# Kernel optimization log

Hardware: AMD Instinct MI355X
Metric: run time of the kernel (lower is better)

The kernel has to match this reference:

```python
import jax, jax.numpy as jnp
import numpy as np
from jax import lax

DIM = 256
HEADS = 8


def dwconv3x3(x, w, b):
    # x: [B,C,H,W], w: [C,1,3,3] depthwise (groups=C), b: [C]
    y = lax.conv_general_dilated(
        x, w, window_strides=(1, 1), padding='SAME',
        dimension_numbers=('NCHW', 'OIHW', 'NCHW'),
        feature_group_count=x.shape[1])
    return y + b[None, :, None, None]


def conv1x1(x, w, b):
    # x: [B,Cin,H,W], w: [Cout,Cin], b: [Cout]
    return jnp.einsum('oc,bchw->bohw', w, x) + b[None, :, None, None]


def setup_inputs() -> dict:
    key = jax.random.key(0)
    ks = jax.random.split(key, 12)
    s = 0.05
    inp = {
        'x': jax.random.normal(ks[0], (4, DIM, 128, 128), dtype=jnp.float32),
        'q_w': jax.random.normal(ks[1], (DIM, 1, 3, 3), dtype=jnp.float32) * s,
        'q_b': jax.random.normal(ks[2], (DIM,), dtype=jnp.float32) * s,
        'k_w': jax.random.normal(ks[3], (DIM, 1, 3, 3), dtype=jnp.float32) * s,
        'k_b': jax.random.normal(ks[4], (DIM,), dtype=jnp.float32) * s,
        'v_w': jax.random.normal(ks[5], (DIM, 1, 3, 3), dtype=jnp.float32) * s,
        'v_b': jax.random.normal(ks[6], (DIM,), dtype=jnp.float32) * s,
        'out_w': jax.random.normal(ks[7], (DIM, DIM), dtype=jnp.float32) * s,
        'out_b': jax.random.normal(ks[8], (DIM,), dtype=jnp.float32) * s,
        'fusion_w': jax.random.normal(ks[9], (DIM, 2 * DIM), dtype=jnp.float32) * s,
        'fusion_b': jax.random.normal(ks[10], (DIM,), dtype=jnp.float32) * s,
        'temperature': jnp.ones((HEADS, 1, 1), dtype=jnp.float32),
        'gamma': jax.random.normal(ks[11], (1,), dtype=jnp.float32) * 0.1,
    }
    return inp


def reference(x, q_w, q_b, k_w, k_b, v_w, v_b, out_w, out_b,
              fusion_w, fusion_b, temperature, gamma):
    b, c, h, w = x.shape
    ch = c // HEADS  # channels per head (32)
    q = dwconv3x3(x, q_w, q_b).reshape(b, HEADS, ch, h * w)
    k = dwconv3x3(x, k_w, k_b).reshape(b, HEADS, ch, h * w)
    v = dwconv3x3(x, v_w, v_b).reshape(b, HEADS, ch, h * w)
    # channel-wise attention: [b, head, c, c]
    attn = jnp.einsum('bhcn,bhdn->bhcd', q, k) * temperature[None]
    attn = jax.nn.softmax(attn, axis=-1)
    out = jnp.einsum('bhcd,bhdn->bhcn', attn, v).reshape(b, c, h, w)
    out = conv1x1(out, out_w, out_b)
    fused = jnp.concatenate([out * gamma[0], x], axis=1)  # [b, 2c, h, w]
    return conv1x1(fused, fusion_w, fusion_b)
```

## Files before the change

kernel.cpp:

```cpp
#include <hip/hip_runtime.h>

typedef __attribute__((ext_vector_type(8))) short bf16x8;
typedef __attribute__((ext_vector_type(4))) float f32x4;

static __device__ __forceinline__ unsigned short f2bf(float f) {
  unsigned u = __builtin_bit_cast(unsigned, f);
  unsigned r = u + 0x7fffu + ((u >> 16) & 1u);
  return (unsigned short)(r >> 16);
}
static __device__ __forceinline__ unsigned pkbf(float a, float b) {
  return (unsigned)f2bf(a) | ((unsigned)f2bf(b) << 16);
}

#define GLOAD_LDS16(g, l)                                              \
  __builtin_amdgcn_global_load_lds(                                    \
      (const __attribute__((address_space(1))) void*)(g),              \
      (__attribute__((address_space(3))) void*)(l), 16, 0, 0)

struct SmA { float xs[4][324]; unsigned short qk[2][32][256]; };
union SmU { SmA a; unsigned short vx[256][72]; };

__global__ __launch_bounds__(256, 4) void k_qkv(
    const float* __restrict__ x,
    const float* __restrict__ q_w, const float* __restrict__ q_b,
    const float* __restrict__ k_w, const float* __restrict__ k_b,
    const float* __restrict__ v_w, const float* __restrict__ v_b,
    unsigned short* __restrict__ bx,
    float* __restrict__ gp)
{
  __shared__ SmU sm;
  const int lin = blockIdx.x + 64 * (blockIdx.y + 8 * blockIdx.z);
  const int nl = ((lin & 7) << 8) | (lin >> 3);
  const int t = nl & 63, h = (nl >> 6) & 7, b = nl >> 9;
  const int tid = threadIdx.x;
  __builtin_assume(tid < 256);
  const int wv = tid >> 6, lane = tid & 63;
  const int w4 = __builtin_amdgcn_readfirstlane(wv);
  const int ty = t >> 3, tx = t & 7;
  const int y0 = ty * 16, x0 = tx * 16;
  const int py = lane >> 2, px0 = (lane & 3) * 4;

  int goff[6];
  #pragma unroll
  for (int k = 0; k < 6; ++k) {
    int r = lane + 64 * k;
    int yy = r / 18, xx = r - yy * 18;
    int gy = y0 + yy - 1, gx = x0 + xx - 1;
    goff[k] = ((r < 324) && ((unsigned)gy < 128u) && ((unsigned)gx < 128u))
                  ? (gy * 128 + gx) : -1;
  }
  const float* cb = x + ((size_t)(b * 256 + h * 32 + w4 * 4)) * 16384;
  float hc[6], hn[6];
  #pragma unroll
  for (int k = 0; k < 6; ++k) { hc[k] = 0.f; if (goff[k] >= 0) hc[k] = cb[goff[k]]; }

  float* xw = &sm.a.xs[w4][0];
  uint2 vpack[2][4], xpack[2][4];
  #pragma unroll
  for (int pass = 0; pass < 2; ++pass) {
    const int cbase = h * 32 + pass * 16;
    #pragma unroll
    for (int j = 0; j < 4; ++j) {
      #pragma unroll
      for (int k = 0; k < 6; ++k) {
        int r = lane + 64 * k;
        if (r < 324) xw[r] = hc[k];
      }
      const bool last = (pass == 1) && (j == 3);
      const int nrel = (j < 3) ? (pass * 16 + j + 1) : 16;
      if (!last) {
        const float* np = cb + (size_t)nrel * 16384;
        #pragma unroll
        for (int k = 0; k < 6; ++k) { hn[k] = 0.f; if (goff[k] >= 0) hn[k] = np[goff[k]]; }
      }
      const int ch = cbase + w4 * 4 + j;
      float wq[9], wk[9], wvv[9];
      #pragma unroll
      for (int i2 = 0; i2 < 9; ++i2) {
        wq[i2]  = q_w[ch * 9 + i2];
        wk[i2]  = k_w[ch * 9 + i2];
        wvv[i2] = v_w[ch * 9 + i2];
      }
      const float bq = q_b[ch], bk = k_b[ch], bv = v_b[ch];
      float aq[4], ak[4], av[4], xr[4];
      #pragma unroll
      for (int px = 0; px < 4; ++px) { aq[px] = bq; ak[px] = bk; av[px] = bv; xr[px] = 0.f; }
      #pragma unroll
      for (int r = 0; r < 3; ++r) {
        const float* xrow = &xw[(py + r) * 18 + px0];
        float2 a01 = *(const float2*)&xrow[0];
        float2 a23 = *(const float2*)&xrow[2];
        float2 a45 = *(const float2*)&xrow[4];
        float rw[6];
        rw[0] = a01.x; rw[1] = a01.y; rw[2] = a23.x;
        rw[3] = a23.y; rw[4] = a45.x; rw[5] = a45.y;
        #pragma unroll
        for (int px = 0; px < 4; ++px) {
          #pragma unroll
          for (int cx = 0; cx < 3; ++cx) {
            float xv = rw[px + cx];
            aq[px] += wq[r * 3 + cx] * xv;
            ak[px] += wk[r * 3 + cx] * xv;
            av[px] += wvv[r * 3 + cx] * xv;
          }
        }
        if (r == 1) {
          #pragma unroll
          for (int px = 0; px < 4; ++px) xr[px] = rw[px + 1];
        }
      }
      const int ah = pass * 16 + w4 * 4 + j;
      const int sw = (((lane >> 1) ^ (ah & 7)) << 3) + ((lane & 1) << 2);
      *(uint2*)&sm.a.qk[0][ah][sw] = make_uint2(pkbf(aq[0], aq[1]), pkbf(aq[2], aq[3]));
      *(uint2*)&sm.a.qk[1][ah][sw] = make_uint2(pkbf(ak[0], ak[1]), pkbf(ak[2], ak[3]));
      #pragma unroll
      for (int px = 0; px < 4; ++px) {
        unsigned fv = (unsigned)f2bf(av[px]);
        unsigned fx = (unsigned)f2bf(xr[px]);
        if (j == 0)      { vpack[pass][px].x = fv;        xpack[pass][px].x = fx; }
        else if (j == 1) { vpack[pass][px].x |= fv << 16; xpack[pass][px].x |= fx << 16; }
        else if (j == 2) { vpack[pass][px].y = fv;        xpack[pass][px].y = fx; }
        else             { vpack[pass][px].y |= fv << 16; xpack[pass][px].y |= fx << 16; }
      }
      if (!last) {
        #pragma unroll
        for (int k = 0; k < 6; ++k) hc[k] = hn[k];
      }
    }
  }
  __syncthreads();

  const int qm = wv >> 1, qn = wv & 1;
  const int lrow = lane & 15, quad = lane >> 4;
  const int rowa = qm * 16 + lrow, rowb = qn * 16 + lrow;
  f32x4 acc = {0.f, 0.f, 0.f, 0.f};
  #pragma unroll
  for (int ks = 0; ks < 8; ++ks) {
    bf16x8 a  = *(const bf16x8*)&sm.a.qk[0][rowa][(((ks * 4 + quad) ^ (rowa & 7)) << 3)];
    bf16x8 bb = *(const bf16x8*)&sm.a.qk[1][rowb][(((ks * 4 + quad) ^ (rowb & 7)) << 3)];
    acc = __builtin_amdgcn_mfma_f32_16x16x32_bf16(a, bb, acc, 0, 0, 0);
  }
  float* gpb = gp + ((size_t)((b * 8 + h) * 64 + t)) * 1024;
  #pragma unroll
  for (int r = 0; r < 4; ++r)
    gpb[(qm * 16 + quad * 4 + r) * 32 + qn * 16 + lrow] = acc[r];

  __syncthreads();

  const int chi = wv >> 1, half = wv & 1;
  #pragma unroll
  for (int pass = 0; pass < 2; ++pass)
    #pragma unroll
    for (int px = 0; px < 4; ++px) {
      int n = py * 16 + px0 + px;
      int key = (n >> 3) & 7;
      int cv = pass * 2 + chi;
      int cx2 = 4 + pass * 2 + chi;
      *(uint2*)&sm.vx[n][((cv ^ key) << 3) + (half << 2)] = vpack[pass][px];
      *(uint2*)&sm.vx[n][((cx2 ^ key) << 3) + (half << 2)] = xpack[pass][px];
    }
  __syncthreads();

  #pragma unroll
  for (int it = 0; it < 8; ++it) {
    int n = it * 32 + (tid >> 3);
    int m = tid & 7;
    int key = (n >> 3) & 7;
    uint4 val = *(const uint4*)&sm.vx[n][((m ^ key) << 3)];
    int pyn = n >> 4, pxn = n & 15;
    int ng = (y0 + pyn) * 128 + x0 + pxn;
    *(uint4*)&bx[((size_t)b * 16384 + ng) * 512 + h * 64 + m * 8] = val;
  }
}

__global__ __launch_bounds__(256) void k_rs_prep(
    const float* __restrict__ gp, const float* __restrict__ temp,
    float* __restrict__ attn,
    const float* __restrict__ out_w, const float* __restrict__ out_b,
    const float* __restrict__ fusion_w, const float* __restrict__ fusion_b,
    const float* __restrict__ gamma,
    float* __restrict__ W1g, float* __restrict__ bias_tot,
    unsigned short* __restrict__ Wcat) {
  const int bi = blockIdx.x;
  const int tid = threadIdx.x;

  if (bi >= 128) {
    const int o = bi - 128;
    const int c = tid;
    const float g = gamma[0];
    float acc = 0.f, bacc = 0.f;
    #pragma unroll 8
    for (int t = 0; t < 256; ++t) {
      float fw = fusion_w[o*512 + t];
      acc  += fw * out_w[t*256 + c];
      bacc += fw * out_b[t];
    }
    W1g[o*256 + c] = g * acc;
    if (c == 0) bias_tot[o] = g * bacc + fusion_b[o];
    unsigned short w2b = f2bf(fusion_w[o*512 + 256 + c]);
    const int col = ((c >> 5) << 6) + 32 + (c & 31);
    for (int b = 0; b < 4; ++b)
      Wcat[((size_t)(b*256 + o))*512 + col] = w2b;
    return;
  }

  const int cs = bi & 3, h = (bi >> 2) & 7, b = bi >> 5;
  const int lc = tid >> 5, d = tid & 31;
  const int c = cs * 8 + lc;
  const float* base = gp + ((size_t)((b*8 + h)*64))*1024 + c*32 + d;
  float s = 0.f;
  #pragma unroll
  for (int g = 0; g < 8; ++g) {
    float p = 0.f;
    #pragma unroll
    for (int i = 0; i < 8; ++i) p += base[(size_t)(g*8 + i)*1024];
    s += p;
  }
  s *= temp[h];
  float m = s;
  #pragma unroll
  for (int off = 16; off; off >>= 1) m = fmaxf(m, __shfl_xor(m, off));
  float e = __expf(s - m);
  float sum = e;
  #pragma unroll
  for (int off = 16; off; off >>= 1) sum += __shfl_xor(sum, off);
  attn[((size_t)((b*8 + h)*32 + c))*32 + d] = e / sum;
}

__global__ __launch_bounds__(256) void k_compose(
    const float* __restrict__ W1g, const float* __restrict__ attn,
    unsigned short* __restrict__ Wcat) {
  const int o = blockIdx.x, b = blockIdx.y;
  const int e = threadIdx.x;
  const int h = e >> 5, d = e & 31;
  const float* ab = attn + ((size_t)((b*8 + h)*32))*32 + d;
  const float* wb = W1g + o*256 + h*32;
  float s = 0.f;
  #pragma unroll
  for (int c2 = 0; c2 < 32; ++c2) s += wb[c2] * ab[c2*32];
  Wcat[((size_t)(b*256 + o))*512 + ((e >> 5) << 6) + (e & 31)] = f2bf(s);
}

__global__ __launch_bounds__(256) void k_gemm(
    const unsigned short* __restrict__ Wcat,
    const unsigned short* __restrict__ bx,
    const float* __restrict__ bias_tot,
    float* __restrict__ out) {
  __shared__ unsigned short Al[2][256][32];
  __shared__ unsigned short Bl[2][64][32];
  const int nt = blockIdx.x, b = blockIdx.y;
  const int tid = threadIdx.x;
  const int wv = tid >> 6, lane = tid & 63;
  const int lrow = lane & 15, quad = lane >> 4;
  const int nbase = nt * 64;
  const unsigned short* Ab = Wcat + (size_t)b * 256 * 512;
  const unsigned short* Bb = bx + ((size_t)b * 16384 + nbase) * 512;
  f32x4 acc[4][4] = {};

  const int srow = tid >> 2;
  const int sq4 = tid & 3;
  const unsigned short* apr = Ab + (size_t)srow * 512 + sq4 * 8;
  const unsigned short* bpr = Bb + (size_t)srow * 512 + sq4 * 8;

  #pragma unroll
  for (int g = 0; g < 4; ++g)
    GLOAD_LDS16(apr + (size_t)g * 64 * 512, &Al[0][wv * 16 + g * 64][0]);
  GLOAD_LDS16(bpr, &Bl[0][wv * 16][0]);
  __syncthreads();

  for (int ks = 0; ks < 16; ++ks) {
    const int cur = ks & 1;
    if (ks < 15) {
      const int k0 = (ks + 1) * 32;
      const int nxt = cur ^ 1;
      #pragma unroll
      for (int g = 0; g < 4; ++g)
        GLOAD_LDS16(apr + (size_t)g * 64 * 512 + k0, &Al[nxt][wv * 16 + g * 64][0]);
      GLOAD_LDS16(bpr + k0, &Bl[nxt][wv * 16][0]);
    }
    bf16x8 af[4], bfv[4];
    #pragma unroll
    for (int i = 0; i < 4; ++i)
      af[i] = *(const bf16x8*)&Al[cur][wv * 64 + i * 16 + lrow][quad * 8];
    #pragma unroll
    for (int j = 0; j < 4; ++j)
      bfv[j] = *(const bf16x8*)&Bl[cur][j * 16 + lrow][quad * 8];
    #pragma unroll
    for (int i = 0; i < 4; ++i)
      #pragma unroll
      for (int j = 0; j < 4; ++j)
        acc[i][j] = __builtin_amdgcn_mfma_f32_16x16x32_bf16(af[i], bfv[j], acc[i][j], 0, 0, 0);
    __syncthreads();
  }

  #pragma unroll
  for (int i = 0; i < 4; ++i) {
    #pragma unroll
    for (int r = 0; r < 4; ++r) {
      const int o = wv*64 + i*16 + quad*4 + r;
      const float bias = bias_tot[o];
      #pragma unroll
      for (int j = 0; j < 4; ++j) {
        const int n = nbase + j*16 + lrow;
        out[((size_t)(b*256 + o))*16384 + n] = acc[i][j][r] + bias;
      }
    }
  }
}

extern "C" void kernel_launch(void* const* d_in, const int* in_sizes, int n_in,
                              void* d_out, int out_size, void* d_ws, size_t ws_size,
                              hipStream_t stream) {
  const float* x        = (const float*)d_in[0];
  const float* q_w      = (const float*)d_in[1];
  const float* q_b      = (const float*)d_in[2];
  const float* k_w      = (const float*)d_in[3];
  const float* k_b      = (const float*)d_in[4];
  const float* v_w      = (const float*)d_in[5];
  const float* v_b      = (const float*)d_in[6];
  const float* out_w    = (const float*)d_in[7];
  const float* out_b    = (const float*)d_in[8];
  const float* fusion_w = (const float*)d_in[9];
  const float* fusion_b = (const float*)d_in[10];
  const float* temp     = (const float*)d_in[11];
  const float* gamma    = (const float*)d_in[12];
  float* out = (float*)d_out;

  char* ws = (char*)d_ws;
  unsigned short* bx   = (unsigned short*)(ws);
  float* gp            = (float*)(ws + 67108864);
  float* attn          = (float*)(ws + 75497472);
  float* W1g           = (float*)(ws + 75628544);
  float* bias_tot      = (float*)(ws + 75890688);
  unsigned short* Wcat = (unsigned short*)(ws + 75891712);

  k_qkv<<<dim3(64, 8, 4), dim3(256), 0, stream>>>(x, q_w, q_b, k_w, k_b, v_w, v_b, bx, gp);
  k_rs_prep<<<dim3(384), dim3(256), 0, stream>>>(gp, temp, attn,
                                                 out_w, out_b, fusion_w, fusion_b,
                                                 gamma, W1g, bias_tot, Wcat);
  k_compose<<<dim3(256, 4), dim3(256), 0, stream>>>(W1g, attn, Wcat);
  k_gemm<<<dim3(256, 4), dim3(256), 0, stream>>>(Wcat, bx, bias_tot, out);
}
```

Measured before the change: 246.1 us.

## Compute V depthwise conv inside final GEMM instead of materializing bf16 V/x buffer

The first kernel no longer computes V or writes the interleaved bf16 V/x buffer (64 MB of workspace writes and reads). The final GEMM now builds its B tiles on the fly, reading fp32 x directly and computing the V depthwise 3x3 conv with wave shuffles for horizontal neighbours. This removes a large intermediate round trip through memory. In exchange the GEMM does conv arithmetic and scattered, less coalesced fp32 loads inside its main loop, which can stall the MFMA pipeline.

```diff
diff --git a/kernel.cpp b/kernel.cpp
--- a/kernel.cpp
+++ b/kernel.cpp
@@ -17,18 +17,15 @@
       (const __attribute__((address_space(1))) void*)(g),              \
       (__attribute__((address_space(3))) void*)(l), 16, 0, 0)
 
-struct SmA { float xs[4][324]; unsigned short qk[2][32][256]; };
-union SmU { SmA a; unsigned short vx[256][72]; };
-
-__global__ __launch_bounds__(256, 4) void k_qkv(
+struct SmQ { float xs[4][324]; unsigned short qk[2][32][256]; };
+
+__global__ __launch_bounds__(256, 3) void k_qk(
     const float* __restrict__ x,
     const float* __restrict__ q_w, const float* __restrict__ q_b,
     const float* __restrict__ k_w, const float* __restrict__ k_b,
-    const float* __restrict__ v_w, const float* __restrict__ v_b,
-    unsigned short* __restrict__ bx,
     float* __restrict__ gp)
 {
-  __shared__ SmU sm;
+  __shared__ SmQ sm;
   const int lin = blockIdx.x + 64 * (blockIdx.y + 8 * blockIdx.z);
   const int nl = ((lin & 7) << 8) | (lin >> 3);
   const int t = nl & 63, h = (nl >> 6) & 7, b = nl >> 9;
@@ -54,8 +51,7 @@
   #pragma unroll
   for (int k = 0; k < 6; ++k) { hc[k] = 0.f; if (goff[k] >= 0) hc[k] = cb[goff[k]]; }
 
-  float* xw = &sm.a.xs[w4][0];
-  uint2 vpack[2][4], xpack[2][4];
+  float* xw = &sm.xs[w4][0];
   #pragma unroll
   for (int pass = 0; pass < 2; ++pass) {
     const int cbase = h * 32 + pass * 16;
@@ -74,17 +70,16 @@
         for (int k = 0; k < 6; ++k) { hn[k] = 0.f; if (goff[k] >= 0) hn[k] = np[goff[k]]; }
       }
       const int ch = cbase + w4 * 4 + j;
-      float wq[9], wk[9], wvv[9];
+      float wq[9], wk[9];
       #pragma unroll
       for (int i2 = 0; i2 < 9; ++i2) {
-        wq[i2]  = q_w[ch * 9 + i2];
-        wk[i2]  = k_w[ch * 9 + i2];
-        wvv[i2] = v_w[ch * 9 + i2];
-      }
-      const float bq = q_b[ch], bk = k_b[ch], bv = v_b[ch];
-      float aq[4], ak[4], av[4], xr[4];
-      #pragma unroll
-      for (int px = 0; px < 4; ++px) { aq[px] = bq; ak[px] = bk; av[px] = bv; xr[px] = 0.f; }
+        wq[i2] = q_w[ch * 9 + i2];
+        wk[i2] = k_w[ch * 9 + i2];
+      }
+      const float bq = q_b[ch], bk = k_b[ch];
+      float aq[4], ak[4];
+      #pragma unroll
+      for (int px = 0; px < 4; ++px) { aq[px] = bq; ak[px] = bk; }
       #pragma unroll
       for (int r = 0; r < 3; ++r) {
         const float* xrow = &xw[(py + r) * 18 + px0];
@@ -95,33 +90,18 @@
         rw[0] = a01.x; rw[1] = a01.y; rw[2] = a23.x;
         rw[3] = a23.y; rw[4] = a45.x; rw[5] = a45.y;
         #pragma unroll
-        for (int px = 0; px < 4; ++px) {
+        for (int px = 0; px < 4; ++px)
           #pragma unroll
           for (int cx = 0; cx < 3; ++cx) {
             float xv = rw[px + cx];
             aq[px] += wq[r * 3 + cx] * xv;
             ak[px] += wk[r * 3 + cx] * xv;
-            av[px] += wvv[r * 3 + cx] * xv;
           }
-        }
-        if (r == 1) {
-          #pragma unroll
-          for (int px = 0; px < 4; ++px) xr[px] = rw[px + 1];
-        }
       }
       const int ah = pass * 16 + w4 * 4 + j;
       const int sw = (((lane >> 1) ^ (ah & 7)) << 3) + ((lane & 1) << 2);
-      *(uint2*)&sm.a.qk[0][ah][sw] = make_uint2(pkbf(aq[0], aq[1]), pkbf(aq[2], aq[3]));
-      *(uint2*)&sm.a.qk[1][ah][sw] = make_uint2(pkbf(ak[0], ak[1]), pkbf(ak[2], ak[3]));
-      #pragma unroll
-      for (int px = 0; px < 4; ++px) {
-        unsigned fv = (unsigned)f2bf(av[px]);
-        unsigned fx = (unsigned)f2bf(xr[px]);
-        if (j == 0)      { vpack[pass][px].x = fv;        xpack[pass][px].x = fx; }
-        else if (j == 1) { vpack[pass][px].x |= fv << 16; xpack[pass][px].x |= fx << 16; }
-        else if (j == 2) { vpack[pass][px].y = fv;        xpack[pass][px].y = fx; }
-        else             { vpack[pass][px].y |= fv << 16; xpack[pass][px].y |= fx << 16; }
-      }
+      *(uint2*)&sm.qk[0][ah][sw] = make_uint2(pkbf(aq[0], aq[1]), pkbf(aq[2], aq[3]));
+      *(uint2*)&sm.qk[1][ah][sw] = make_uint2(pkbf(ak[0], ak[1]), pkbf(ak[2], ak[3]));
       if (!last) {
         #pragma unroll
         for (int k = 0; k < 6; ++k) hc[k] = hn[k];
@@ -136,41 +116,14 @@
   f32x4 acc = {0.f, 0.f, 0.f, 0.f};
   #pragma unroll
   for (int ks = 0; ks < 8; ++ks) {
-    bf16x8 a  = *(const bf16x8*)&sm.a.qk[0][rowa][(((ks * 4 + quad) ^ (rowa & 7)) << 3)];
-    bf16x8 bb = *(const bf16x8*)&sm.a.qk[1][rowb][(((ks * 4 + quad) ^ (rowb & 7)) << 3)];
+    bf16x8 a  = *(const bf16x8*)&sm.qk[0][rowa][(((ks * 4 + quad) ^ (rowa & 7)) << 3)];
+    bf16x8 bb = *(const bf16x8*)&sm.qk[1][rowb][(((ks * 4 + quad) ^ (rowb & 7)) << 3)];
     acc = __builtin_amdgcn_mfma_f32_16x16x32_bf16(a, bb, acc, 0, 0, 0);
   }
   float* gpb = gp + ((size_t)((b * 8 + h) * 64 + t)) * 1024;
   #pragma unroll
   for (int r = 0; r < 4; ++r)
     gpb[(qm * 16 + quad * 4 + r) * 32 + qn * 16 + lrow] = acc[r];
-
-  __syncthreads();
-
-  const int chi = wv >> 1, half = wv & 1;
-  #pragma unroll
-  for (int pass = 0; pass < 2; ++pass)
-    #pragma unroll
-    for (int px = 0; px < 4; ++px) {
-      int n = py * 16 + px0 + px;
-      int key = (n >> 3) & 7;
-      int cv = pass * 2 + chi;
-      int cx2 = 4 + pass * 2 + chi;
-      *(uint2*)&sm.vx[n][((cv ^ key) << 3) + (half << 2)] = vpack[pass][px];
-      *(uint2*)&sm.vx[n][((cx2 ^ key) << 3) + (half << 2)] = xpack[pass][px];
-    }
-  __syncthreads();
-
-  #pragma unroll
-  for (int it = 0; it < 8; ++it) {
-    int n = it * 32 + (tid >> 3);
-    int m = tid & 7;
-    int key = (n >> 3) & 7;
-    uint4 val = *(const uint4*)&sm.vx[n][((m ^ key) << 3)];
-    int pyn = n >> 4, pxn = n & 15;
-    int ng = (y0 + pyn) * 128 + x0 + pxn;
-    *(uint4*)&bx[((size_t)b * 16384 + ng) * 512 + h * 64 + m * 8] = val;
-  }
 }
 
 __global__ __launch_bounds__(256) void k_rs_prep(
@@ -241,9 +194,57 @@
   Wcat[((size_t)(b*256 + o))*512 + ((e >> 5) << 6) + (e & 31)] = f2bf(s);
 }
 
-__global__ __launch_bounds__(256) void k_gemm(
+static __device__ __forceinline__ void stage_B(
+    const float* __restrict__ x, const float* __restrict__ v_w,
+    const float* __restrict__ v_b, int b, int nbase, int tid, int s,
+    unsigned short (*__restrict__ Blb)[32]) {
+  const int wq = tid >> 6, n = tid & 63;
+  const int ng = nbase + n;
+  const int chb = (s >> 1) * 32 + wq * 8;
+  unsigned pk0, pk1, pk2, pk3;
+  if (s & 1) {
+    const float* xp = x + ((size_t)(b * 256 + chb)) * 16384 + ng;
+    pk0 = pkbf(xp[0],           xp[16384]);
+    pk1 = pkbf(xp[2 * 16384],   xp[3 * 16384]);
+    pk2 = pkbf(xp[4 * 16384],   xp[5 * 16384]);
+    pk3 = pkbf(xp[6 * 16384],   xp[7 * 16384]);
+  } else {
+    const int y = ng >> 7, xc = ng & 127;
+    float av8[8];
+    #pragma unroll
+    for (int u = 0; u < 8; ++u) {
+      const int ch = chb + u;
+      const float* wp = v_w + ch * 9;
+      const float* rp = x + ((size_t)(b * 256 + ch)) * 16384 + xc;
+      float av = v_b[ch];
+      #pragma unroll
+      for (int dy = 0; dy < 3; ++dy) {
+        const int gy = y + dy - 1;
+        if ((unsigned)gy < 128u) {
+          const float* row = rp + gy * 128;
+          float xm = row[0];
+          float xl = __shfl_up(xm, 1);
+          float xr = __shfl_down(xm, 1);
+          if (n == 0)  xl = (xc > 0)   ? row[-1] : 0.f;
+          if (n == 63) xr = (xc < 127) ? row[1]  : 0.f;
+          av += wp[dy * 3 + 0] * xl;
+          av += wp[dy * 3 + 1] * xm;
+          av += wp[dy * 3 + 2] * xr;
+        }
+      }
+      av8[u] = av;
+    }
+    pk0 = pkbf(av8[0], av8[1]); pk1 = pkbf(av8[2], av8[3]);
+    pk2 = pkbf(av8[4], av8[5]); pk3 = pkbf(av8[6], av8[7]);
+  }
+  const int key = (n ^ (n >> 2)) & 3;
+  *(uint4*)&Blb[n][((wq ^ key) << 3)] = make_uint4(pk0, pk1, pk2, pk3);
+}
+
+__global__ __launch_bounds__(256) void k_gx(
     const unsigned short* __restrict__ Wcat,
-    const unsigned short* __restrict__ bx,
+    const float* __restrict__ x,
+    const float* __restrict__ v_w, const float* __restrict__ v_b,
     const float* __restrict__ bias_tot,
     float* __restrict__ out) {
   __shared__ unsigned short Al[2][256][32];
@@ -254,18 +255,16 @@
   const int lrow = lane & 15, quad = lane >> 4;
   const int nbase = nt * 64;
   const unsigned short* Ab = Wcat + (size_t)b * 256 * 512;
-  const unsigned short* Bb = bx + ((size_t)b * 16384 + nbase) * 512;
   f32x4 acc[4][4] = {};
 
   const int srow = tid >> 2;
   const int sq4 = tid & 3;
   const unsigned short* apr = Ab + (size_t)srow * 512 + sq4 * 8;
-  const unsigned short* bpr = Bb + (size_t)srow * 512 + sq4 * 8;
 
   #pragma unroll
   for (int g = 0; g < 4; ++g)
     GLOAD_LDS16(apr + (size_t)g * 64 * 512, &Al[0][wv * 16 + g * 64][0]);
-  GLOAD_LDS16(bpr, &Bl[0][wv * 16][0]);
+  stage_B(x, v_w, v_b, b, nbase, tid, 0, Bl[0]);
   __syncthreads();
 
   for (int ks = 0; ks < 16; ++ks) {
@@ -276,15 +275,18 @@
       #pragma unroll
       for (int g = 0; g < 4; ++g)
         GLOAD_LDS16(apr + (size_t)g * 64 * 512 + k0, &Al[nxt][wv * 16 + g * 64][0]);
-      GLOAD_LDS16(bpr + k0, &Bl[nxt][wv * 16][0]);
+      stage_B(x, v_w, v_b, b, nbase, tid, ks + 1, Bl[nxt]);
     }
     bf16x8 af[4], bfv[4];
     #pragma unroll
     for (int i = 0; i < 4; ++i)
       af[i] = *(const bf16x8*)&Al[cur][wv * 64 + i * 16 + lrow][quad * 8];
     #pragma unroll
-    for (int j = 0; j < 4; ++j)
-      bfv[j] = *(const bf16x8*)&Bl[cur][j * 16 + lrow][quad * 8];
+    for (int j = 0; j < 4; ++j) {
+      const int row = j * 16 + lrow;
+      const int key = (row ^ (row >> 2)) & 3;
+      bfv[j] = *(const bf16x8*)&Bl[cur][row][((quad ^ key) << 3)];
+    }
     #pragma unroll
     for (int i = 0; i < 4; ++i)
       #pragma unroll
@@ -327,17 +329,16 @@
   float* out = (float*)d_out;
 
   char* ws = (char*)d_ws;
-  unsigned short* bx   = (unsigned short*)(ws);
-  float* gp            = (float*)(ws + 67108864);
-  float* attn          = (float*)(ws + 75497472);
-  float* W1g           = (float*)(ws + 75628544);
-  float* bias_tot      = (float*)(ws + 75890688);
-  unsigned short* Wcat = (unsigned short*)(ws + 75891712);
-
-  k_qkv<<<dim3(64, 8, 4), dim3(256), 0, stream>>>(x, q_w, q_b, k_w, k_b, v_w, v_b, bx, gp);
+  float* gp            = (float*)(ws);
+  float* attn          = (float*)(ws + 8388608);
+  float* W1g           = (float*)(ws + 8519680);
+  float* bias_tot      = (float*)(ws + 8781824);
+  unsigned short* Wcat = (unsigned short*)(ws + 8782848);
+
+  k_qk<<<dim3(64, 8, 4), dim3(256), 0, stream>>>(x, q_w, q_b, k_w, k_b, gp);
   k_rs_prep<<<dim3(384), dim3(256), 0, stream>>>(gp, temp, attn,
                                                  out_w, out_b, fusion_w, fusion_b,
                                                  gamma, W1g, bias_tot, Wcat);
   k_compose<<<dim3(256, 4), dim3(256), 0, stream>>>(W1g, attn, Wcat);
-  k_gemm<<<dim3(256, 4), dim3(256), 0, stream>>>(Wcat, bx, bias_tot, out);
-}
+  k_gx<<<dim3(256, 4), dim3(256), 0, stream>>>(Wcat, x, v_w, v_b, bias_tot, out);
+}
```

Measured after the change: 433.9 us. +76.3%, slower.
